# Kernel tuning notes

Hardware: AMD Instinct MI355X
Metric: run time of the kernel (lower is better)

## Reference

```python
import jax, jax.numpy as jnp
import numpy as np

B, LH, LU, H = 32, 1024, 128, 256
NEG = -1e30


def setup_inputs() -> dict:
    key = jax.random.key(0)
    k1, k2, k3, k4, k5, k6 = jax.random.split(key, 6)
    h = jax.random.normal(k1, (B, LH, H), jnp.float32)
    u = jax.random.normal(k2, (B, LU, H), jnp.float32)
    # valid-prefix padding masks (at least half the sequence valid)
    h_len = jax.random.randint(k3, (B,), LH // 2, LH + 1)
    u_len = jax.random.randint(k4, (B,), LU // 2, LU + 1)
    h_mask = jnp.arange(LH)[None, :] < h_len[:, None]
    u_mask = jnp.arange(LU)[None, :] < u_len[:, None]
    # sim_proj: Linear(3H, 1) -> weight flattened to [3H], scalar bias
    w = jax.random.normal(k5, (3 * H,), jnp.float32) / np.sqrt(3 * H)
    b = jax.random.normal(k6, (), jnp.float32)
    return {"h": h, "u": u, "h_mask": h_mask, "u_mask": u_mask, "w": w, "b": b}


def reference(h, u, h_mask, u_mask, w, b):
    d = h.shape[-1]
    w_h, w_u, w_hu = w[:d], w[d:2 * d], w[2 * d:]
    # S[b,i,j] = [h_i; u_j; h_i*u_j] @ w + b  (decomposed, no [B,Lh,Lu,3H] blow-up)
    S = ((h @ w_h)[:, :, None]
         + (u @ w_u)[:, None, :]
         + jnp.einsum('bih,bjh->bij', h * w_hu, u)
         + b)  # [B, Lh, Lu]
    neg = jnp.asarray(NEG, S.dtype)
    # context-to-query attention: softmax over u (dim 2), masked by u_mask
    a_t = jax.nn.softmax(jnp.where(u_mask[:, None, :], S, neg), axis=2)  # [B,Lh,Lu]
    U_tilde = jnp.einsum('bij,bjh->bih', a_t, u)  # [B,Lh,H]
    # query-to-context attention: softmax over h (dim 1), masked by h_mask
    b_t = jax.nn.softmax(jnp.where(h_mask[:, :, None], S, neg), axis=1)  # [B,Lh,Lu]
    b2 = jnp.einsum('biu,bju->bij', b_t, a_t)  # [B,Lh,Lh] = b_t @ a_t^T
    H_tilde = jnp.einsum('bij,bjh->bih', b2, h)  # [B,Lh,H]
    return jnp.concatenate([h, U_tilde, h * U_tilde, h * H_tilde], axis=-1)
```

## Files before the change

### kernel.cpp

```cpp
#include <hip/hip_runtime.h>
#include <hip/hip_bf16.h>

#define BB  32
#define LHH 1024
#define LUU 128
#define HDD 256
#define NEGF (-1e30f)

typedef __attribute__((ext_vector_type(8))) short short8;
typedef __attribute__((ext_vector_type(4))) short short4v;
typedef __attribute__((ext_vector_type(4))) float f32x4;

static constexpr size_t P_OFF    = 0;
static constexpr size_t UWBP_OFF = P_OFF + (size_t)BB*LHH*LUU/2;
static constexpr size_t RM_OFF   = UWBP_OFF + (size_t)BB*8*LUU;
static constexpr size_t RI_OFF   = RM_OFF + (size_t)BB*LHH;
static constexpr size_t PM_OFF   = RI_OFF + (size_t)BB*LHH;
static constexpr size_t PS_OFF   = PM_OFF + (size_t)BB*16*LUU;
static constexpr size_t CM_OFF   = PS_OFF + (size_t)BB*16*LUU;
static constexpr size_t CI_OFF   = CM_OFF + (size_t)BB*LUU;
static constexpr size_t UBT_OFF  = CI_OFF + (size_t)BB*LUU;
static constexpr size_t CBT_OFF  = UBT_OFF + (size_t)BB*HDD*LUU/2;
static constexpr size_t VBF_OFF  = CBT_OFF + (size_t)BB*HDD*LUU/2;
static constexpr size_t FLAG_OFF = VBF_OFF + (size_t)BB*LUU*HDD/2;
static constexpr size_t WS_FLOATS= FLAG_OFF + 1;

__device__ __forceinline__ float mval(const void* p, int idx, int flag) {
    if (flag) return ((const unsigned char*)p)[idx] ? 1.0f : 0.0f;
    return (((const int*)p)[idx] != 0) ? 1.0f : 0.0f;
}
__device__ __forceinline__ float cexpf(float x) { return __expf(fminf(x, 60.0f)); }
__device__ __forceinline__ float grcp(float x)  { return 1.0f / fmaxf(x, 1e-38f); }
__device__ __forceinline__ int swz(int r) { return (r ^ (r >> 2)) & 3; }
__device__ __forceinline__ float b2f(short v) {
    return __uint_as_float(((unsigned)(unsigned short)v) << 16);
}
__device__ __forceinline__ short f2b(float x) {
    __hip_bfloat16 h = __float2bfloat16(x);
    return *reinterpret_cast<short*>(&h);
}

__global__ __launch_bounds__(256) void k_prep(const float* __restrict__ u,
                                              const float* __restrict__ w,
                                              const unsigned char* __restrict__ hm,
                                              float* __restrict__ ws) {
    __shared__ float ls[32][132];
    int b = blockIdx.x, hd0 = blockIdx.y * 32;
    int t = threadIdx.x;
    if (blockIdx.x == 0 && blockIdx.y == 0 && t == 0)
        reinterpret_cast<int*>(ws)[FLAG_OFF] = (hm[1] != 0) ? 1 : 0;
    int hc = t & 7, jj = t >> 3;
    float4 whv  = *reinterpret_cast<const float4*>(w + hd0 + hc * 4);
    float4 wuv  = *reinterpret_cast<const float4*>(w + HDD + hd0 + hc * 4);
    float4 whuv = *reinterpret_cast<const float4*>(w + 2 * HDD + hd0 + hc * 4);
    short* vbf = reinterpret_cast<short*>(ws + VBF_OFF);
    #pragma unroll
    for (int pass = 0; pass < 4; ++pass) {
        int j = jj + pass * 32;
        float4 v = *reinterpret_cast<const float4*>(u + ((size_t)(b * LUU + j)) * HDD + hd0 + hc * 4);
        ls[hc * 4 + 0][j] = v.x; ls[hc * 4 + 1][j] = v.y;
        ls[hc * 4 + 2][j] = v.z; ls[hc * 4 + 3][j] = v.w;
        union { short4v s4; __hip_bfloat16 bh[4]; } pv;
        pv.bh[0] = __float2bfloat16(whv.x + whuv.x * v.x);
        pv.bh[1] = __float2bfloat16(whv.y + whuv.y * v.y);
        pv.bh[2] = __float2bfloat16(whv.z + whuv.z * v.z);
        pv.bh[3] = __float2bfloat16(whv.w + whuv.w * v.w);
        *reinterpret_cast<short4v*>(&vbf[((size_t)(b * LUU + j)) * HDD + hd0 + hc * 4]) = pv.s4;
        float s = v.x * wuv.x + v.y * wuv.y + v.z * wuv.z + v.w * wuv.w;
        s += __shfl_xor(s, 1); s += __shfl_xor(s, 2); s += __shfl_xor(s, 4);
        if (hc == 0) ws[UWBP_OFF + (b * 8 + blockIdx.y) * LUU + j] = s;
    }
    __syncthreads();
    int r = t >> 3, ck = t & 7;
    short* ubt = reinterpret_cast<short*>(ws + UBT_OFF);
    union { short8 s8; __hip_bfloat16 bh[8]; } pk;
    #pragma unroll
    for (int hhalf = 0; hhalf < 2; ++hhalf) {
        #pragma unroll
        for (int c = 0; c < 8; ++c)
            pk.bh[c] = __float2bfloat16(ls[r][ck * 16 + hhalf * 8 + c]);
        *reinterpret_cast<short8*>(&ubt[((size_t)(b * 256 + hd0 + r)) * 128 + ck * 16 + hhalf * 8]) = pk.s8;
    }
}

__global__ __launch_bounds__(256) void k_Smfma(const float* __restrict__ h,
                                               const void* __restrict__ u_mask,
                                               const void* __restrict__ h_mask,
                                               const float* __restrict__ bias,
                                               float* __restrict__ ws) {
    __shared__ __align__(16) short lh[64 * 32];
    __shared__ __align__(16) short lv[128 * 32];
    __shared__ float uwb_l[128], um_l[128], hm_l[64];
    __shared__ float credm[4][128], creds[4][128];

    int b  = blockIdx.x;
    int i0 = blockIdx.y * 64;
    int t  = threadIdx.x;
    int flag = reinterpret_cast<const int*>(ws)[FLAG_OFF];
    int wave = t >> 6, lane = t & 63;
    int lj = lane & 15, lq = lane >> 4;

    if (t < 128) {
        float s = bias[0];
        #pragma unroll
        for (int c = 0; c < 8; ++c) s += ws[UWBP_OFF + (b * 8 + c) * LUU + t];
        uwb_l[t] = s;
        um_l[t]  = mval(u_mask, b * LUU + t, flag);
    } else if (t < 192) {
        hm_l[t - 128] = mval(h_mask, b * LHH + i0 + (t - 128), flag);
    }

    int hrow = t >> 2,  hc = t & 3,  hlc = hc ^ swz(hrow);
    int vrow0 = t >> 2, vc0 = t & 3, vlc0 = vc0 ^ swz(vrow0);
    int vrow1 = (t + 256) >> 2, vc1 = t & 3, vlc1 = vc1 ^ swz(vrow1);
    const float* hsrc = h + ((size_t)(b * LHH + i0 + hrow)) * HDD + hlc * 8;
    const short* vbf  = reinterpret_cast<const short*>(ws + VBF_OFF);
    const short* vsrc0 = vbf + ((size_t)(b * LUU + vrow0)) * HDD + vlc0 * 8;
    const short* vsrc1 = vbf + ((size_t)(b * LUU + vrow1)) * HDD + vlc1 * 8;

    int arow = wave * 16 + lj;
    int a_idx = arow * 32 + ((lq ^ swz(arow)) * 8);
    int b_idx[8];
    #pragma unroll
    for (int n = 0; n < 8; ++n) {
        int j = n * 16 + lj;
        b_idx[n] = j * 32 + ((lq ^ swz(j)) * 8);
    }

    f32x4 acc[8];
    #pragma unroll
    for (int n = 0; n < 8; ++n) acc[n] = (f32x4){0.f, 0.f, 0.f, 0.f};

    for (int step = 0; step < 8; ++step) {
        int k0 = step * 32;
        if (step) __syncthreads();
        {
            float4 f0 = *reinterpret_cast<const float4*>(hsrc + k0);
            float4 f1 = *reinterpret_cast<const float4*>(hsrc + k0 + 4);
            union { short8 s8; __hip_bfloat16 bh[8]; } pk;
            pk.bh[0]=__float2bfloat16(f0.x); pk.bh[1]=__float2bfloat16(f0.y);
            pk.bh[2]=__float2bfloat16(f0.z); pk.bh[3]=__float2bfloat16(f0.w);
            pk.bh[4]=__float2bfloat16(f1.x); pk.bh[5]=__float2bfloat16(f1.y);
            pk.bh[6]=__float2bfloat16(f1.z); pk.bh[7]=__float2bfloat16(f1.w);
            *reinterpret_cast<short8*>(&lh[hrow * 32 + hc * 8]) = pk.s8;
        }
        *reinterpret_cast<short8*>(&lv[vrow0 * 32 + vc0 * 8]) =
            *reinterpret_cast<const short8*>(vsrc0 + k0);
        *reinterpret_cast<short8*>(&lv[vrow1 * 32 + vc1 * 8]) =
            *reinterpret_cast<const short8*>(vsrc1 + k0);
        __syncthreads();
        short8 af = *reinterpret_cast<const short8*>(&lh[a_idx]);
        #pragma unroll
        for (int n = 0; n < 8; ++n) {
            short8 bf = *reinterpret_cast<const short8*>(&lv[b_idx[n]]);
            acc[n] = __builtin_amdgcn_mfma_f32_16x16x32_bf16(af, bf, acc[n], 0, 0, 0);
        }
    }

    float sv[8][4];
    #pragma unroll
    for (int n = 0; n < 8; ++n) {
        float uw = uwb_l[n * 16 + lj];
        #pragma unroll
        for (int q = 0; q < 4; ++q) sv[n][q] = acc[n][q] + uw;
    }
    float umv[8];
    #pragma unroll
    for (int n = 0; n < 8; ++n) umv[n] = um_l[n * 16 + lj];

    short* Pg = reinterpret_cast<short*>(ws + P_OFF);
    #pragma unroll
    for (int q = 0; q < 4; ++q) {
        float ms = NEGF;
        #pragma unroll
        for (int n = 0; n < 8; ++n) ms = fmaxf(ms, umv[n] > 0.f ? sv[n][q] : NEGF);
        #pragma unroll
        for (int off = 8; off; off >>= 1) ms = fmaxf(ms, __shfl_xor(ms, off));
        float pe[8], e = 0.f;
        #pragma unroll
        for (int n = 0; n < 8; ++n) { pe[n] = cexpf(sv[n][q] - ms); e += umv[n] * pe[n]; }
        #pragma unroll
        for (int off = 8; off; off >>= 1) e += __shfl_xor(e, off);
        int i = i0 + wave * 16 + lq * 4 + q;
        short* Prow = Pg + ((size_t)(b * LHH + i)) * LUU;
        #pragma unroll
        for (int n = 0; n < 8; ++n) Prow[n * 16 + lj] = f2b(pe[n]);
        if (lj == 0) {
            ws[RM_OFF + b * LHH + i] = ms;
            ws[RI_OFF + b * LHH + i] = grcp(e);
        }
    }

    float hmq[4];
    #pragma unroll
    for (int q = 0; q < 4; ++q) hmq[q] = hm_l[wave * 16 + lq * 4 + q];
    #pragma unroll
    for (int n = 0; n < 8; ++n) {
        float cmx = NEGF, csx = 0.f;
        #pragma unroll
        for (int q = 0; q < 4; ++q) {
            if (hmq[q] > 0.f) {
                float x  = sv[n][q];
                float mn = fmaxf(cmx, x);
                csx = csx * cexpf(cmx - mn) + cexpf(x - mn);
                cmx = mn;
            }
        }
        #pragma unroll
        for (int off = 16; off <= 32; off <<= 1) {
            float om = __shfl_xor(cmx, off);
            float os = __shfl_xor(csx, off);
            float mn = fmaxf(cmx, om);
            csx = csx * cexpf(cmx - mn) + os * cexpf(om - mn);
            cmx = mn;
        }
        if (lq == 0) { credm[wave][n * 16 + lj] = cmx; creds[wave][n * 16 + lj] = csx; }
    }
    __syncthreads();
    if (t < 128) {
        float m = credm[0][t], s = creds[0][t];
        #pragma unroll
        for (int wv = 1; wv < 4; ++wv) {
            float om = credm[wv][t], os = creds[wv][t];
            float mn = fmaxf(m, om);
            s = s * cexpf(m - mn) + os * cexpf(om - mn);
            m = mn;
        }
        ws[PM_OFF + (b * 16 + blockIdx.y) * LUU + t] = m;
        ws[PS_OFF + (b * 16 + blockIdx.y) * LUU + t] = s;
    }
}

__global__ __launch_bounds__(256) void k_Cmfma(const float* __restrict__ h,
                                               const void* __restrict__ u_mask,
                                               float* __restrict__ ws) {
    __shared__ __align__(16) short lha[128 * 32];
    __shared__ __align__(16) short lsa[64 * 32];
    __shared__ float um_s[64];
    int b = blockIdx.x, hd0 = blockIdx.y * 128, u0 = blockIdx.z * 64;
    int t = threadIdx.x;
    int flag = reinterpret_cast<const int*>(ws)[FLAG_OFF];

    if (t < 64) um_s[t] = mval(u_mask, b * LUU + u0 + t, flag);

    if (blockIdx.y == 0 && blockIdx.z == 0 && t >= 64 && t < 192) {
        int j = t - 64;
        float m = NEGF;
        #pragma unroll
        for (int c = 0; c < 16; ++c) m = fmaxf(m, ws[PM_OFF + (b * 16 + c) * LUU + j]);
        float s = 0.f;
        #pragma unroll
        for (int c = 0; c < 16; ++c)
            s += ws[PS_OFF + (b * 16 + c) * LUU + j] * cexpf(ws[PM_OFF + (b * 16 + c) * LUU + j] - m);
        ws[CM_OFF + b * LUU + j] = m;
        ws[CI_OFF + b * LUU + j] = grcp(s);
    }

    int wave = t >> 6, lane = t & 63, lj = lane & 15, lq = lane >> 4;
    int hd_r = t & 127, ah = t >> 7;
    int u_r = t & 63, bc = t >> 6;
    const float* hbp = h + (size_t)b * LHH * HDD + hd0 + hd_r;
    const short* Pbp = reinterpret_cast<const short*>(ws + P_OFF) + (size_t)b * LHH * LUU + u0 + u_r;
    const float* ri = ws + RI_OFF + b * LHH;

    int a_idx[2], b_idx[4];
    #pragma unroll
    for (int m = 0; m < 2; ++m) {
        int row = wave * 32 + m * 16 + lj;
        a_idx[m] = row * 32 + ((lq ^ swz(row)) * 8);
    }
    #pragma unroll
    for (int n = 0; n < 4; ++n) {
        int row = n * 16 + lj;
        b_idx[n] = row * 32 + ((lq ^ swz(row)) * 8);
    }

    f32x4 acc[2][4];
    #pragma unroll
    for (int m = 0; m < 2; ++m)
        #pragma unroll
        for (int n = 0; n < 4; ++n) acc[m][n] = (f32x4){0.f, 0.f, 0.f, 0.f};

    for (int step = 0; step < 32; ++step) {
        int i0 = step * 32;
        if (step) __syncthreads();
        #pragma unroll
        for (int cc = 0; cc < 2; ++cc) {
            int c = ah * 2 + cc, p = c ^ swz(hd_r);
            union { short8 s8; __hip_bfloat16 bh[8]; } pk;
            #pragma unroll
            for (int e = 0; e < 8; ++e)
                pk.bh[e] = __float2bfloat16(hbp[(size_t)(i0 + c * 8 + e) * HDD]);
            *reinterpret_cast<short8*>(&lha[hd_r * 32 + p * 8]) = pk.s8;
        }
        {
            int c = bc, p = c ^ swz(u_r);
            union { short8 s8; __hip_bfloat16 bh[8]; } pk;
            #pragma unroll
            for (int e = 0; e < 8; ++e) {
                int i = i0 + c * 8 + e;
                float pv = b2f(Pbp[(size_t)i * LUU]);
                pk.bh[e] = __float2bfloat16(pv * ri[i]);
            }
            *reinterpret_cast<short8*>(&lsa[u_r * 32 + p * 8]) = pk.s8;
        }
        __syncthreads();
        short8 af0 = *reinterpret_cast<const short8*>(&lha[a_idx[0]]);
        short8 af1 = *reinterpret_cast<const short8*>(&lha[a_idx[1]]);
        #pragma unroll
        for (int n = 0; n < 4; ++n) {
            short8 bf = *reinterpret_cast<const short8*>(&lsa[b_idx[n]]);
            acc[0][n] = __builtin_amdgcn_mfma_f32_16x16x32_bf16(af0, bf, acc[0][n], 0, 0, 0);
            acc[1][n] = __builtin_amdgcn_mfma_f32_16x16x32_bf16(af1, bf, acc[1][n], 0, 0, 0);
        }
    }

    __hip_bfloat16* cbt = reinterpret_cast<__hip_bfloat16*>(ws + CBT_OFF);
    #pragma unroll
    for (int m = 0; m < 2; ++m)
        #pragma unroll
        for (int q = 0; q < 4; ++q) {
            int hd = hd0 + wave * 32 + m * 16 + lq * 4 + q;
            #pragma unroll
            for (int n = 0; n < 4; ++n) {
                int uu = n * 16 + lj;
                cbt[(size_t)(b * 256 + hd) * 128 + u0 + uu] =
                    __float2bfloat16(acc[m][n][q] * um_s[uu]);
            }
        }
}

__global__ __launch_bounds__(256) void k_outm(const float* __restrict__ h,
                                              const void* __restrict__ h_mask,
                                              const void* __restrict__ u_mask,
                                              const float* __restrict__ ws,
                                              float* __restrict__ out) {
    __shared__ __align__(16) short la[64 * 32], lb[64 * 32];
    __shared__ __align__(16) short lu[128 * 32], lc[128 * 32];
    __shared__ float ri_l[64], R_l[64];
    __shared__ float um_l[128], Cc_l[128];

    int b = blockIdx.x, i0 = blockIdx.y * 64, hd0 = blockIdx.z * 128;
    int t = threadIdx.x;
    int flag = reinterpret_cast<const int*>(ws)[FLAG_OFF];
    int wave = t >> 6, lane = t & 63, lj = lane & 15, lq = lane >> 4;

    if (t < 64) {
        float rmv = ws[RM_OFF + b * LHH + i0 + t];
        ri_l[t] = ws[RI_OFF + b * LHH + i0 + t];
        R_l[t]  = mval(h_mask, b * LHH + i0 + t, flag) * cexpf(rmv);
    } else if (t < 192) {
        int j = t - 64;
        float cmv = ws[CM_OFF + b * LUU + j];
        Cc_l[j] = cexpf(-cmv) * ws[CI_OFF + b * LUU + j];
        um_l[j] = mval(u_mask, b * LUU + j, flag);
    }

    const short* Pbase = reinterpret_cast<const short*>(ws + P_OFF) + (size_t)b * LHH * LUU;
    const short* ubt = reinterpret_cast<const short*>(ws + UBT_OFF) + ((size_t)(b * 256 + hd0)) * 128;
    const short* cbt = reinterpret_cast<const short*>(ws + CBT_OFF) + ((size_t)(b * 256 + hd0)) * 128;

    int air = t >> 2, ap = t & 3;
    int brow = t >> 1;
    int a_idx = (wave * 16 + lj) * 32 + ((lq ^ swz(wave * 16 + lj)) * 8);
    int b_idx[8];
    #pragma unroll
    for (int n = 0; n < 8; ++n) {
        int r = n * 16 + lj;
        b_idx[n] = r * 32 + ((lq ^ swz(r)) * 8);
    }

    f32x4 aU[8], aH[8];
    #pragma unroll
    for (int n = 0; n < 8; ++n) { aU[n] = (f32x4){0,0,0,0}; aH[n] = (f32x4){0,0,0,0}; }

    for (int step = 0; step < 4; ++step) {
        int j0 = step * 32;
        __syncthreads();
        {
            int lgc = ap ^ swz(air);
            short8 pv8 = *reinterpret_cast<const short8*>(
                Pbase + (size_t)(i0 + air) * LUU + j0 + lgc * 8);
            float riv = ri_l[air], Rv = R_l[air];
            union { short8 s8; __hip_bfloat16 bh[8]; } pa, pb;
            #pragma unroll
            for (int c = 0; c < 8; ++c) {
                int j = j0 + lgc * 8 + c;
                float p = b2f(pv8[c]);
                pa.bh[c] = __float2bfloat16(p * um_l[j] * riv);
                pb.bh[c] = __float2bfloat16(p * Rv * Cc_l[j]);
            }
            *reinterpret_cast<short8*>(&la[air * 32 + ap * 8]) = pa.s8;
            *reinterpret_cast<short8*>(&lb[air * 32 + ap * 8]) = pb.s8;
        }
        #pragma unroll
        for (int pp = 0; pp < 2; ++pp) {
            int p = (t & 1) * 2 + pp;
            int lgc = p ^ swz(brow);
            *reinterpret_cast<short8*>(&lu[brow * 32 + p * 8]) =
                *reinterpret_cast<const short8*>(ubt + (size_t)brow * 128 + j0 + lgc * 8);
            *reinterpret_cast<short8*>(&lc[brow * 32 + p * 8]) =
                *reinterpret_cast<const short8*>(cbt + (size_t)brow * 128 + j0 + lgc * 8);
        }
        __syncthreads();
        short8 fa = *reinterpret_cast<const short8*>(&la[a_idx]);
        short8 fb = *reinterpret_cast<const short8*>(&lb[a_idx]);
        #pragma unroll
        for (int n = 0; n < 8; ++n) {
            short8 gu = *reinterpret_cast<const short8*>(&lu[b_idx[n]]);
            short8 gc = *reinterpret_cast<const short8*>(&lc[b_idx[n]]);
            aU[n] = __builtin_amdgcn_mfma_f32_16x16x32_bf16(fa, gu, aU[n], 0, 0, 0);
            aH[n] = __builtin_amdgcn_mfma_f32_16x16x32_bf16(fb, gc, aH[n], 0, 0, 0);
        }
    }

    #pragma unroll
    for (int n = 0; n < 8; ++n) {
        int hd = hd0 + n * 16 + lj;
        #pragma unroll
        for (int q = 0; q < 4; ++q) {
            int i = i0 + wave * 16 + lq * 4 + q;
            float hv = h[((size_t)(b * LHH + i)) * HDD + hd];
            size_t base = ((size_t)(b * LHH + i)) * (4 * HDD) + hd;
            float Uv = aU[n][q], Hv = aH[n][q];
            out[base]           = hv;
            out[base + HDD]     = Uv;
            out[base + 2 * HDD] = hv * Uv;
            out[base + 3 * HDD] = hv * Hv;
        }
    }
}

extern "C" void kernel_launch(void* const* d_in, const int* in_sizes, int n_in,
                              void* d_out, int out_size, void* d_ws, size_t ws_size,
                              hipStream_t stream) {
    const float* h = (const float*)d_in[0];
    const float* u = (const float*)d_in[1];
    const void*  h_mask = d_in[2];
    const void*  u_mask = d_in[3];
    const float* w    = (const float*)d_in[4];
    const float* bias = (const float*)d_in[5];
    float* ws  = (float*)d_ws;
    float* out = (float*)d_out;

    if (ws_size < WS_FLOATS * sizeof(float)) return;

    k_prep<<<dim3(BB, HDD / 32), 256, 0, stream>>>(u, w, (const unsigned char*)h_mask, ws);
    k_Smfma<<<dim3(BB, LHH / 64), 256, 0, stream>>>(h, u_mask, h_mask, bias, ws);
    k_Cmfma<<<dim3(BB, 2, 2), 256, 0, stream>>>(h, u_mask, ws);
    k_outm<<<dim3(BB, LHH / 64, 2), 256, 0, stream>>>(h, h_mask, u_mask, ws, out);
}
```

Baseline: 84.75 us.

## Pre-normalize softmax P in S kernel and split C-kernel tiles across more blocks

The S kernel now multiplies P by the row reciprocal before storing it as bf16. That removes the per-element ri scaling in k_Cmfma and k_outm; k_outm instead folds 1/ri into a per-row factor for the H path. k_Cmfma tiles over 64 hidden dims instead of 128, which doubles the grid to 256 blocks for better CU occupancy but means each block reloads P. Storing normalized P in bf16 changes how rounding error is distributed.

```diff
diff --git a/kernel.cpp b/kernel.cpp
--- a/kernel.cpp
+++ b/kernel.cpp
@@ -181,13 +181,14 @@
         for (int n = 0; n < 8; ++n) { pe[n] = cexpf(sv[n][q] - ms); e += umv[n] * pe[n]; }
         #pragma unroll
         for (int off = 8; off; off >>= 1) e += __shfl_xor(e, off);
+        float riv = grcp(e);
         int i = i0 + wave * 16 + lq * 4 + q;
         short* Prow = Pg + ((size_t)(b * LHH + i)) * LUU;
         #pragma unroll
-        for (int n = 0; n < 8; ++n) Prow[n * 16 + lj] = f2b(pe[n]);
+        for (int n = 0; n < 8; ++n) Prow[n * 16 + lj] = f2b(pe[n] * riv);
         if (lj == 0) {
             ws[RM_OFF + b * LHH + i] = ms;
-            ws[RI_OFF + b * LHH + i] = grcp(e);
+            ws[RI_OFF + b * LHH + i] = riv;
         }
     }
 
@@ -234,10 +235,10 @@
 __global__ __launch_bounds__(256) void k_Cmfma(const float* __restrict__ h,
                                                const void* __restrict__ u_mask,
                                                float* __restrict__ ws) {
-    __shared__ __align__(16) short lha[128 * 32];
+    __shared__ __align__(16) short lha[64 * 32];
     __shared__ __align__(16) short lsa[64 * 32];
     __shared__ float um_s[64];
-    int b = blockIdx.x, hd0 = blockIdx.y * 128, u0 = blockIdx.z * 64;
+    int b = blockIdx.x, hd0 = blockIdx.y * 64, u0 = blockIdx.z * 64;
     int t = threadIdx.x;
     int flag = reinterpret_cast<const int*>(ws)[FLAG_OFF];
 
@@ -257,77 +258,63 @@
     }
 
     int wave = t >> 6, lane = t & 63, lj = lane & 15, lq = lane >> 4;
-    int hd_r = t & 127, ah = t >> 7;
+    int hd_r = t >> 2, ac = t & 3;
     int u_r = t & 63, bc = t >> 6;
     const float* hbp = h + (size_t)b * LHH * HDD + hd0 + hd_r;
     const short* Pbp = reinterpret_cast<const short*>(ws + P_OFF) + (size_t)b * LHH * LUU + u0 + u_r;
-    const float* ri = ws + RI_OFF + b * LHH;
-
-    int a_idx[2], b_idx[4];
-    #pragma unroll
-    for (int m = 0; m < 2; ++m) {
-        int row = wave * 32 + m * 16 + lj;
-        a_idx[m] = row * 32 + ((lq ^ swz(row)) * 8);
-    }
+
+    int arow = wave * 16 + lj;
+    int a_idx = arow * 32 + ((lq ^ swz(arow)) * 8);
+    int b_idx[4];
     #pragma unroll
     for (int n = 0; n < 4; ++n) {
         int row = n * 16 + lj;
         b_idx[n] = row * 32 + ((lq ^ swz(row)) * 8);
     }
 
-    f32x4 acc[2][4];
-    #pragma unroll
-    for (int m = 0; m < 2; ++m)
-        #pragma unroll
-        for (int n = 0; n < 4; ++n) acc[m][n] = (f32x4){0.f, 0.f, 0.f, 0.f};
+    f32x4 acc[4];
+    #pragma unroll
+    for (int n = 0; n < 4; ++n) acc[n] = (f32x4){0.f, 0.f, 0.f, 0.f};
 
     for (int step = 0; step < 32; ++step) {
         int i0 = step * 32;
         if (step) __syncthreads();
-        #pragma unroll
-        for (int cc = 0; cc < 2; ++cc) {
-            int c = ah * 2 + cc, p = c ^ swz(hd_r);
+        {
+            int p = ac ^ swz(hd_r);
             union { short8 s8; __hip_bfloat16 bh[8]; } pk;
             #pragma unroll
             for (int e = 0; e < 8; ++e)
-                pk.bh[e] = __float2bfloat16(hbp[(size_t)(i0 + c * 8 + e) * HDD]);
+                pk.bh[e] = __float2bfloat16(hbp[(size_t)(i0 + ac * 8 + e) * HDD]);
             *reinterpret_cast<short8*>(&lha[hd_r * 32 + p * 8]) = pk.s8;
         }
         {
-            int c = bc, p = c ^ swz(u_r);
-            union { short8 s8; __hip_bfloat16 bh[8]; } pk;
+            int p = bc ^ swz(u_r);
+            short8 pk;
             #pragma unroll
-            for (int e = 0; e < 8; ++e) {
-                int i = i0 + c * 8 + e;
-                float pv = b2f(Pbp[(size_t)i * LUU]);
-                pk.bh[e] = __float2bfloat16(pv * ri[i]);
-            }
-            *reinterpret_cast<short8*>(&lsa[u_r * 32 + p * 8]) = pk.s8;
+            for (int e = 0; e < 8; ++e)
+                pk[e] = Pbp[(size_t)(i0 + bc * 8 + e) * LUU];
+            *reinterpret_cast<short8*>(&lsa[u_r * 32 + p * 8]) = pk;
         }
         __syncthreads();
-        short8 af0 = *reinterpret_cast<const short8*>(&lha[a_idx[0]]);
-        short8 af1 = *reinterpret_cast<const short8*>(&lha[a_idx[1]]);
+        short8 af = *reinterpret_cast<const short8*>(&lha[a_idx]);
         #pragma unroll
         for (int n = 0; n < 4; ++n) {
             short8 bf = *reinterpret_cast<const short8*>(&lsa[b_idx[n]]);
-            acc[0][n] = __builtin_amdgcn_mfma_f32_16x16x32_bf16(af0, bf, acc[0][n], 0, 0, 0);
-            acc[1][n] = __builtin_amdgcn_mfma_f32_16x16x32_bf16(af1, bf, acc[1][n], 0, 0, 0);
+            acc[n] = __builtin_amdgcn_mfma_f32_16x16x32_bf16(af, bf, acc[n], 0, 0, 0);
         }
     }
 
     __hip_bfloat16* cbt = reinterpret_cast<__hip_bfloat16*>(ws + CBT_OFF);
     #pragma unroll
-    for (int m = 0; m < 2; ++m)
-        #pragma unroll
-        for (int q = 0; q < 4; ++q) {
-            int hd = hd0 + wave * 32 + m * 16 + lq * 4 + q;
-            #pragma unroll
-            for (int n = 0; n < 4; ++n) {
-                int uu = n * 16 + lj;
-                cbt[(size_t)(b * 256 + hd) * 128 + u0 + uu] =
-                    __float2bfloat16(acc[m][n][q] * um_s[uu]);
-            }
-        }
+    for (int q = 0; q < 4; ++q) {
+        int hd = hd0 + wave * 16 + lq * 4 + q;
+        #pragma unroll
+        for (int n = 0; n < 4; ++n) {
+            int uu = n * 16 + lj;
+            cbt[(size_t)(b * 256 + hd) * 128 + u0 + uu] =
+                __float2bfloat16(acc[n][q] * um_s[uu]);
+        }
+    }
 }
 
 __global__ __launch_bounds__(256) void k_outm(const float* __restrict__ h,
@@ -337,7 +324,7 @@
                                               float* __restrict__ out) {
     __shared__ __align__(16) short la[64 * 32], lb[64 * 32];
     __shared__ __align__(16) short lu[128 * 32], lc[128 * 32];
-    __shared__ float ri_l[64], R_l[64];
+    __shared__ float R2_l[64];
     __shared__ float um_l[128], Cc_l[128];
 
     int b = blockIdx.x, i0 = blockIdx.y * 64, hd0 = blockIdx.z * 128;
@@ -347,8 +334,8 @@
 
     if (t < 64) {
         float rmv = ws[RM_OFF + b * LHH + i0 + t];
-        ri_l[t] = ws[RI_OFF + b * LHH + i0 + t];
-        R_l[t]  = mval(h_mask, b * LHH + i0 + t, flag) * cexpf(rmv);
+        float riv = ws[RI_OFF + b * LHH + i0 + t];
+        R2_l[t] = mval(h_mask, b * LHH + i0 + t, flag) * cexpf(rmv) / riv;
     } else if (t < 192) {
         int j = t - 64;
         float cmv = ws[CM_OFF + b * LUU + j];
@@ -381,14 +368,14 @@
             int lgc = ap ^ swz(air);
             short8 pv8 = *reinterpret_cast<const short8*>(
                 Pbase + (size_t)(i0 + air) * LUU + j0 + lgc * 8);
-            float riv = ri_l[air], Rv = R_l[air];
+            float R2v = R2_l[air];
             union { short8 s8; __hip_bfloat16 bh[8]; } pa, pb;
             #pragma unroll
             for (int c = 0; c < 8; ++c) {
                 int j = j0 + lgc * 8 + c;
                 float p = b2f(pv8[c]);
-                pa.bh[c] = __float2bfloat16(p * um_l[j] * riv);
-                pb.bh[c] = __float2bfloat16(p * Rv * Cc_l[j]);
+                pa.bh[c] = __float2bfloat16(p * um_l[j]);
+                pb.bh[c] = __float2bfloat16(p * R2v * Cc_l[j]);
             }
             *reinterpret_cast<short8*>(&la[air * 32 + ap * 8]) = pa.s8;
             *reinterpret_cast<short8*>(&lb[air * 32 + ap * 8]) = pb.s8;
@@ -447,6 +434,6 @@
 
     k_prep<<<dim3(BB, HDD / 32), 256, 0, stream>>>(u, w, (const unsigned char*)h_mask, ws);
     k_Smfma<<<dim3(BB, LHH / 64), 256, 0, stream>>>(h, u_mask, h_mask, bias, ws);
-    k_Cmfma<<<dim3(BB, 2, 2), 256, 0, stream>>>(h, u_mask, ws);
+    k_Cmfma<<<dim3(BB, 4, 2), 256, 0, stream>>>(h, u_mask, ws);
     k_outm<<<dim3(BB, LHH / 64, 2), 256, 0, stream>>>(h, h_mask, u_mask, ws, out);
 }
```

New measurement: 83.99 us, median of 2. Within noise of the previous version (-0.9%).
